# Kernel optimization log

Hardware: AMD Instinct MI355X
Metric: run time of the kernel (lower is better)

## Reference

```python
import jax, jax.numpy as jnp
import numpy as np

B, S, D = 2, 4096, 1024

def setup_inputs() -> dict:
    key = jax.random.key(0)
    k1, k2 = jax.random.split(key)
    x = jax.random.normal(k1, (B, S, D), dtype=jnp.float32)
    W = jax.random.normal(k2, (D, 3 * D), dtype=jnp.float32) * (1.0 / np.sqrt(D))
    b = jnp.zeros((3 * D,), dtype=jnp.float32)
    return {"x": x, "W": W, "b": b}

def reference(x, W, b) -> jnp.ndarray:
    D_ = x.shape[-1]
    qkv = x @ W + b                       # [B, S, 3D]
    q, k, v = jnp.split(qkv, 3, axis=2)    # each [B, S, D]
    scale = 1.0 / jnp.sqrt(jnp.asarray(D_, dtype=x.dtype))
    scores = jnp.einsum('bqd,bkd->bqk', q, k) * scale  # [B, S, S]
    weights = jax.nn.softmax(scores, axis=-1)
    return jnp.einsum('bqk,bkd->bqd', weights, v)       # [B, S, D]
```

## Files before the change

kernel.cpp:

```cpp
#include <hip/hip_runtime.h>
#include <hip/hip_bf16.h>

typedef __attribute__((ext_vector_type(4))) float  f32x4;
typedef __attribute__((ext_vector_type(8))) __bf16 bf16x8;
typedef __attribute__((ext_vector_type(8))) unsigned short u16x8;

typedef const __attribute__((address_space(1))) void gas_void;
typedef __attribute__((address_space(3))) void las_void;

__device__ __forceinline__ unsigned short f2bf(float x) {
    unsigned u = __builtin_bit_cast(unsigned, x);
    u += 0x7fffu + ((u >> 16) & 1u);
    return (unsigned short)(u >> 16);
}
__device__ __forceinline__ float bf2f(unsigned short h) {
    unsigned u = ((unsigned)h) << 16;
    return __builtin_bit_cast(float, u);
}
__device__ __forceinline__ void gload_lds16(const void* g, void* l) {
    __builtin_amdgcn_global_load_lds((gas_void*)g, (las_void*)l, 16, 0, 0);
}

__global__ void k_f32_to_bf16(const float* __restrict__ in,
                              unsigned short* __restrict__ out, int n4) {
    int i = blockIdx.x * blockDim.x + threadIdx.x;
    if (i < n4) {
        float4 v = ((const float4*)in)[i];
        ushort4 o;
        o.x = f2bf(v.x); o.y = f2bf(v.y); o.z = f2bf(v.z); o.w = f2bf(v.w);
        ((ushort4*)out)[i] = o;
    }
}

__global__ void k_transpose_w(const float* __restrict__ W,
                              unsigned short* __restrict__ Wt,
                              int K, int N) {
    __shared__ unsigned short tile[32][33];
    int n0 = blockIdx.x * 32, k0 = blockIdx.y * 32;
    int tx = threadIdx.x, ty = threadIdx.y;
#pragma unroll
    for (int i = 0; i < 4; i++) {
        int kk = ty + i * 8;
        tile[kk][tx] = f2bf(W[(size_t)(k0 + kk) * N + n0 + tx]);
    }
    __syncthreads();
#pragma unroll
    for (int i = 0; i < 4; i++) {
        int nn = ty + i * 8;
        Wt[(size_t)(n0 + nn) * K + k0 + tx] = tile[tx][nn];
    }
}

__global__ void k_transpose_v(const unsigned short* __restrict__ Vrow,
                              unsigned short* __restrict__ Vt) {
    __shared__ unsigned short tile[32][33];
    int b = blockIdx.z;
    int s0 = blockIdx.x * 32, d0 = blockIdx.y * 32;
    int tx = threadIdx.x, ty = threadIdx.y;
#pragma unroll
    for (int i = 0; i < 4; i++) {
        int ss = ty + i * 8;
        tile[ss][tx] = Vrow[((size_t)(b * 4096 + s0 + ss)) * 1024 + d0 + tx];
    }
    __syncthreads();
#pragma unroll
    for (int i = 0; i < 4; i++) {
        int dd = ty + i * 8;
        Vt[((size_t)b * 1024 + d0 + dd) * 4096 + s0 + tx] = tile[tx][dd];
    }
}

template <int MODE>
__global__ void k_gemm_bt(const unsigned short* __restrict__ A, int lda,
                          const unsigned short* __restrict__ Bt, int ldb,
                          void* __restrict__ C, int ldc,
                          unsigned short* __restrict__ Vp,
                          const float* __restrict__ bias,
                          int K, float alpha,
                          long sA, long sB, long sC) {
    __shared__ __align__(16) unsigned short As[128 * 32];
    __shared__ __align__(16) unsigned short Bs[128 * 32];

    const int z = blockIdx.z;
    A  += (size_t)z * sA;
    Bt += (size_t)z * sB;

    const int tid  = threadIdx.x;
    const int lane = tid & 63;
    const int w    = tid >> 6;
    const int wr   = w >> 1, wc = w & 1;
    const int m0   = blockIdx.y * 128;
    const int n0   = blockIdx.x * 128;

    f32x4 acc[4][4] = {};

    const int r0  = lane >> 2;
    const int cEl = (lane & 3) * 8;

    for (int k0 = 0; k0 < K; k0 += 32) {
#pragma unroll
        for (int i = 0; i < 2; i++) {
            const int c   = w + 4 * i;
            const int row = c * 16 + r0;
            gload_lds16(A + (size_t)(m0 + row) * lda + k0 + cEl,
                        (void*)(As + c * 512));
        }
#pragma unroll
        for (int i = 0; i < 2; i++) {
            const int c   = w + 4 * i;
            const int row = c * 16 + r0;
            gload_lds16(Bt + (size_t)(n0 + row) * ldb + k0 + cEl,
                        (void*)(Bs + c * 512));
        }
        __syncthreads();

        bf16x8 af[4], bfr[4];
#pragma unroll
        for (int m = 0; m < 4; m++)
            af[m] = *(const bf16x8*)&As[(wr * 64 + m * 16 + (lane & 15)) * 32 + (lane >> 4) * 8];
#pragma unroll
        for (int n = 0; n < 4; n++)
            bfr[n] = *(const bf16x8*)&Bs[(wc * 64 + n * 16 + (lane & 15)) * 32 + (lane >> 4) * 8];

#pragma unroll
        for (int m = 0; m < 4; m++)
#pragma unroll
            for (int n = 0; n < 4; n++)
                acc[m][n] = __builtin_amdgcn_mfma_f32_16x16x32_bf16(af[m], bfr[n], acc[m][n], 0, 0, 0);

        __syncthreads();
    }

#pragma unroll
    for (int m = 0; m < 4; m++) {
        const int row = m0 + wr * 64 + m * 16 + (lane >> 4) * 4;
#pragma unroll
        for (int n = 0; n < 4; n++) {
            const int col = n0 + wc * 64 + n * 16 + (lane & 15);
            const float bv = (MODE == 2) ? bias[col] : 0.0f;
#pragma unroll
            for (int r = 0; r < 4; r++) {
                const float v = acc[m][n][r] * alpha + bv;
                if (MODE == 0) {
                    ((float*)C)[(size_t)z * sC + (size_t)(row + r) * ldc + col] = v;
                } else if (MODE == 1) {
                    ((unsigned short*)C)[(size_t)z * sC + (size_t)(row + r) * ldc + col] = f2bf(v);
                } else {
                    const int lc = col & 1023;
                    if (col < 2048) {
                        ((unsigned short*)C)[(size_t)(col >> 10) * 8388608 +
                                             (size_t)(row + r) * 1024 + lc] = f2bf(v);
                    } else {
                        Vp[(size_t)(row + r) * 1024 + lc] = f2bf(v);
                    }
                }
            }
        }
    }
}

__global__ __launch_bounds__(256) void k_softmax_inplace(unsigned short* __restrict__ P, int S) {
    __shared__ float red[8];
    const int row  = blockIdx.x;
    const int tid  = threadIdx.x;
    const int lane = tid & 63;
    const int wid  = tid >> 6;
    unsigned short* p = P + (size_t)row * S;

    float v[16];
    u16x8 h0 = *(const u16x8*)&p[tid * 16];
    u16x8 h1 = *(const u16x8*)&p[tid * 16 + 8];
    float mx = -1e30f;
#pragma unroll
    for (int j = 0; j < 8; j++) { v[j]     = bf2f(h0[j]); mx = fmaxf(mx, v[j]);     }
#pragma unroll
    for (int j = 0; j < 8; j++) { v[j + 8] = bf2f(h1[j]); mx = fmaxf(mx, v[j + 8]); }

#pragma unroll
    for (int o = 32; o >= 1; o >>= 1) mx = fmaxf(mx, __shfl_xor(mx, o));
    if (lane == 0) red[wid] = mx;
    __syncthreads();
    mx = fmaxf(fmaxf(red[0], red[1]), fmaxf(red[2], red[3]));

    float sum = 0.0f;
#pragma unroll
    for (int j = 0; j < 16; j++) { v[j] = __expf(v[j] - mx); sum += v[j]; }
#pragma unroll
    for (int o = 32; o >= 1; o >>= 1) sum += __shfl_xor(sum, o);
    if (lane == 0) red[4 + wid] = sum;
    __syncthreads();
    sum = red[4] + red[5] + red[6] + red[7];
    const float rinv = 1.0f / sum;

    u16x8 o0, o1;
#pragma unroll
    for (int j = 0; j < 8; j++) { o0[j] = f2bf(v[j] * rinv); o1[j] = f2bf(v[j + 8] * rinv); }
    *(u16x8*)&p[tid * 16]     = o0;
    *(u16x8*)&p[tid * 16 + 8] = o1;
}

extern "C" void kernel_launch(void* const* d_in, const int* in_sizes, int n_in,
                              void* d_out, int out_size, void* d_ws, size_t ws_size,
                              hipStream_t stream) {
    const float* x    = (const float*)d_in[0];
    const float* W    = (const float*)d_in[1];
    const float* bias = (const float*)d_in[2];
    float* out        = (float*)d_out;

    char* ws = (char*)d_ws;
    unsigned short* Qb   = (unsigned short*)(ws);
    unsigned short* Vt   = (unsigned short*)(ws + 33554432);
    unsigned short* xb   = (unsigned short*)(ws + 50331648);
    unsigned short* Wt   = (unsigned short*)(ws + 67108864);
    unsigned short* Vrow = (unsigned short*)(ws + 73400320);
    unsigned short* Pcat = (unsigned short*)(ws + 50331648);

    k_f32_to_bf16<<<8192, 256, 0, stream>>>(x, xb, (8192 * 1024) / 4);
    k_transpose_w<<<dim3(96, 32), dim3(32, 8), 0, stream>>>(W, Wt, 1024, 3072);
    k_gemm_bt<2><<<dim3(24, 64, 1), 256, 0, stream>>>(
        xb, 1024, Wt, 1024, (void*)Qb, 1024, Vrow, bias, 1024, 1.0f, 0, 0, 0);
    k_transpose_v<<<dim3(128, 32, 2), dim3(32, 8), 0, stream>>>(Vrow, Vt);

    const float scale = 0.03125f;
    k_gemm_bt<1><<<dim3(32, 32, 2), 256, 0, stream>>>(
        Qb, 1024, Qb + 8388608, 1024, (void*)Pcat, 4096, nullptr, nullptr,
        1024, scale, 4194304, 4194304, 16777216);
    k_softmax_inplace<<<8192, 256, 0, stream>>>(Pcat, 4096);
    k_gemm_bt<0><<<dim3(8, 32, 2), 256, 0, stream>>>(
        Pcat, 4096, Vt, 4096, (void*)out, 1024, nullptr, nullptr,
        4096, 1.0f, 16777216, 4194304, 4194304);
}
```

Measured before the change: 302.6 us.

## Use 256x256 double-buffered swizzled-LDS GEMM for QKV and score products

```diff
diff --git a/kernel.cpp b/kernel.cpp
--- a/kernel.cpp
+++ b/kernel.cpp
@@ -20,6 +20,8 @@
 __device__ __forceinline__ void gload_lds16(const void* g, void* l) {
     __builtin_amdgcn_global_load_lds((gas_void*)g, (las_void*)l, 16, 0, 0);
 }
+
+#define WAITVM(N) asm volatile("s_waitcnt vmcnt(" #N ")" ::: "memory")
 
 __global__ void k_f32_to_bf16(const float* __restrict__ in,
                               unsigned short* __restrict__ out, int n4) {
@@ -71,45 +73,187 @@
 }
 
 template <int MODE>
-__global__ void k_gemm_bt(const unsigned short* __restrict__ A, int lda,
-                          const unsigned short* __restrict__ Bt, int ldb,
-                          void* __restrict__ C, int ldc,
-                          unsigned short* __restrict__ Vp,
-                          const float* __restrict__ bias,
-                          int K, float alpha,
-                          long sA, long sB, long sC) {
-    __shared__ __align__(16) unsigned short As[128 * 32];
-    __shared__ __align__(16) unsigned short Bs[128 * 32];
+__global__ __launch_bounds__(512, 2) void k_gemm256(
+        const unsigned short* __restrict__ A, int lda,
+        const unsigned short* __restrict__ Bt, int ldb,
+        void* __restrict__ C, int ldc,
+        unsigned short* __restrict__ Vp,
+        const float* __restrict__ bias,
+        int K, float alpha, long sA, long sB, long sC) {
+    __shared__ __align__(16) unsigned short As[2][16384];
+    __shared__ __align__(16) unsigned short Bs[2][16384];
 
     const int z = blockIdx.z;
     A  += (size_t)z * sA;
     Bt += (size_t)z * sB;
+
+    const int nwg  = gridDim.x * gridDim.y;
+    const int flat = blockIdx.y * gridDim.x + blockIdx.x;
+    const int swzb = (flat & 7) * (nwg >> 3) + (flat >> 3);
+    const int m0   = (swzb / gridDim.x) * 256;
+    const int n0   = (swzb % gridDim.x) * 256;
+
+    const int tid  = threadIdx.x;
+    const int lane = tid & 63;
+    const int wid  = tid >> 6;
+    const int wm   = wid >> 2;
+    const int wn   = wid & 3;
+    const int l15  = lane & 15;
+    const int l4   = lane >> 4;
+
+    f32x4 acc[8][4] = {};
+
+    auto stageA = [&](int b, int h, int kt) {
+#pragma unroll
+        for (int c = 0; c < 2; c++) {
+            int phi = c * 8192 + tid * 16;
+            int lam = phi ^ (((phi >> 9) & 1) << 5);
+            int rowp = lam >> 7;
+            int kel  = (lam & 127) >> 1;
+            int grow = m0 + (rowp >> 6) * 128 + h * 64 + (rowp & 63);
+            gload_lds16(A + (size_t)grow * lda + kt * 64 + kel,
+                        (char*)As + b * 32768 + h * 16384 + c * 8192 + (wid << 10));
+        }
+    };
+    auto stageB = [&](int b, int h, int kt) {
+#pragma unroll
+        for (int c = 0; c < 2; c++) {
+            int phi = c * 8192 + tid * 16;
+            int lam = phi ^ (((phi >> 9) & 1) << 5);
+            int rowp = lam >> 7;
+            int kel  = (lam & 127) >> 1;
+            int gnrow = n0 + (rowp >> 5) * 64 + h * 32 + (rowp & 31);
+            gload_lds16(Bt + (size_t)gnrow * ldb + kt * 64 + kel,
+                        (char*)Bs + b * 32768 + h * 16384 + c * 8192 + (wid << 10));
+        }
+    };
+    auto rdA = [&](int b, int qm, int mf, int kk) -> bf16x8 {
+        int rowp = wm * 64 + mf * 16 + l15;
+        int lam  = qm * 16384 + rowp * 128 + kk * 64 + l4 * 16;
+        int ads  = lam ^ (((lam >> 9) & 1) << 5);
+        return *(const bf16x8*)((const char*)As + b * 32768 + ads);
+    };
+    auto rdB = [&](int b, int qn, int nf, int kk) -> bf16x8 {
+        int rowp = wn * 32 + nf * 16 + l15;
+        int lam  = qn * 16384 + rowp * 128 + kk * 64 + l4 * 16;
+        int ads  = lam ^ (((lam >> 9) & 1) << 5);
+        return *(const bf16x8*)((const char*)Bs + b * 32768 + ads);
+    };
+
+#define MM(I, J, X, Y) \
+    acc[I][J] = __builtin_amdgcn_mfma_f32_16x16x32_bf16((X), (Y), acc[I][J], 0, 0, 0)
+
+#define PHASE(BUF, QM, QN, WAIT_STMT, STG_STMT)                                \
+    do {                                                                       \
+        WAIT_STMT;                                                             \
+        __builtin_amdgcn_s_barrier();                                          \
+        __builtin_amdgcn_sched_barrier(0);                                     \
+        STG_STMT;                                                              \
+        bf16x8 a00 = rdA(BUF, QM, 0, 0), a01 = rdA(BUF, QM, 0, 1);             \
+        bf16x8 a10 = rdA(BUF, QM, 1, 0), a11 = rdA(BUF, QM, 1, 1);             \
+        bf16x8 a20 = rdA(BUF, QM, 2, 0), a21 = rdA(BUF, QM, 2, 1);             \
+        bf16x8 a30 = rdA(BUF, QM, 3, 0), a31 = rdA(BUF, QM, 3, 1);             \
+        bf16x8 b00 = rdB(BUF, QN, 0, 0), b01 = rdB(BUF, QN, 0, 1);             \
+        bf16x8 b10 = rdB(BUF, QN, 1, 0), b11 = rdB(BUF, QN, 1, 1);             \
+        __builtin_amdgcn_s_setprio(1);                                         \
+        MM(QM * 4 + 0, QN * 2 + 0, a00, b00); MM(QM * 4 + 0, QN * 2 + 0, a01, b01); \
+        MM(QM * 4 + 0, QN * 2 + 1, a00, b10); MM(QM * 4 + 0, QN * 2 + 1, a01, b11); \
+        MM(QM * 4 + 1, QN * 2 + 0, a10, b00); MM(QM * 4 + 1, QN * 2 + 0, a11, b01); \
+        MM(QM * 4 + 1, QN * 2 + 1, a10, b10); MM(QM * 4 + 1, QN * 2 + 1, a11, b11); \
+        MM(QM * 4 + 2, QN * 2 + 0, a20, b00); MM(QM * 4 + 2, QN * 2 + 0, a21, b01); \
+        MM(QM * 4 + 2, QN * 2 + 1, a20, b10); MM(QM * 4 + 2, QN * 2 + 1, a21, b11); \
+        MM(QM * 4 + 3, QN * 2 + 0, a30, b00); MM(QM * 4 + 3, QN * 2 + 0, a31, b01); \
+        MM(QM * 4 + 3, QN * 2 + 1, a30, b10); MM(QM * 4 + 3, QN * 2 + 1, a31, b11); \
+        __builtin_amdgcn_s_setprio(0);                                         \
+    } while (0)
+
+    const int NT = K >> 6;
+    stageA(0, 0, 0); stageB(0, 0, 0); stageA(0, 1, 0); stageB(0, 1, 0);
+
+    for (int t = 0; t < NT; t++) {
+        const int cb = t & 1, nb = cb ^ 1;
+        if (t + 1 < NT) {
+            PHASE(cb, 0, 0, WAITVM(4), stageA(nb, 0, t + 1));
+            PHASE(cb, 1, 0, WAITVM(4), stageB(nb, 0, t + 1));
+            PHASE(cb, 0, 1, WAITVM(4), stageA(nb, 1, t + 1));
+            PHASE(cb, 1, 1, (void)0,   stageB(nb, 1, t + 1));
+        } else {
+            PHASE(cb, 0, 0, WAITVM(4), (void)0);
+            PHASE(cb, 1, 0, WAITVM(2), (void)0);
+            PHASE(cb, 0, 1, WAITVM(0), (void)0);
+            PHASE(cb, 1, 1, (void)0,   (void)0);
+        }
+    }
+#undef PHASE
+#undef MM
+
+#pragma unroll
+    for (int qm = 0; qm < 2; qm++)
+#pragma unroll
+    for (int mf = 0; mf < 4; mf++) {
+        const int row = m0 + wm * 128 + qm * 64 + mf * 16 + l4 * 4;
+#pragma unroll
+        for (int qn = 0; qn < 2; qn++)
+#pragma unroll
+        for (int nf = 0; nf < 2; nf++) {
+            const int col = n0 + wn * 64 + qn * 32 + nf * 16 + l15;
+            const float bv = (MODE == 2) ? bias[col] : 0.0f;
+            const f32x4 av = acc[qm * 4 + mf][qn * 2 + nf];
+#pragma unroll
+            for (int r = 0; r < 4; r++) {
+                const float v = av[r] * alpha + bv;
+                if (MODE == 1) {
+                    ((unsigned short*)C)[(size_t)z * sC + (size_t)(row + r) * ldc + col] = f2bf(v);
+                } else {
+                    const int lc = col & 1023;
+                    if (col < 2048)
+                        ((unsigned short*)C)[(size_t)(col >> 10) * 8388608 +
+                                             (size_t)(row + r) * 1024 + lc] = f2bf(v);
+                    else
+                        Vp[(size_t)(row + r) * 1024 + lc] = f2bf(v);
+                }
+            }
+        }
+    }
+}
+
+__global__ void k_gemm_bt_f32(const unsigned short* __restrict__ A, int lda,
+                              const unsigned short* __restrict__ Bt, int ldb,
+                              float* __restrict__ C, int ldc,
+                              int K, long sA, long sB, long sC) {
+    __shared__ __align__(16) unsigned short As[128 * 32];
+    __shared__ __align__(16) unsigned short Bs[128 * 32];
+
+    const int z = blockIdx.z;
+    A  += (size_t)z * sA;
+    Bt += (size_t)z * sB;
+
+    const int nwg  = gridDim.x * gridDim.y;
+    const int flat = blockIdx.y * gridDim.x + blockIdx.x;
+    const int swzb = (flat & 7) * (nwg >> 3) + (flat >> 3);
+    const int m0   = (swzb / gridDim.x) * 128;
+    const int n0   = (swzb % gridDim.x) * 128;
 
     const int tid  = threadIdx.x;
     const int lane = tid & 63;
     const int w    = tid >> 6;
     const int wr   = w >> 1, wc = w & 1;
-    const int m0   = blockIdx.y * 128;
-    const int n0   = blockIdx.x * 128;
 
     f32x4 acc[4][4] = {};
-
     const int r0  = lane >> 2;
     const int cEl = (lane & 3) * 8;
 
     for (int k0 = 0; k0 < K; k0 += 32) {
 #pragma unroll
         for (int i = 0; i < 2; i++) {
-            const int c   = w + 4 * i;
-            const int row = c * 16 + r0;
-            gload_lds16(A + (size_t)(m0 + row) * lda + k0 + cEl,
+            const int c = w + 4 * i;
+            gload_lds16(A + (size_t)(m0 + c * 16 + r0) * lda + k0 + cEl,
                         (void*)(As + c * 512));
         }
 #pragma unroll
         for (int i = 0; i < 2; i++) {
-            const int c   = w + 4 * i;
-            const int row = c * 16 + r0;
-            gload_lds16(Bt + (size_t)(n0 + row) * ldb + k0 + cEl,
+            const int c = w + 4 * i;
+            gload_lds16(Bt + (size_t)(n0 + c * 16 + r0) * ldb + k0 + cEl,
                         (void*)(Bs + c * 512));
         }
         __syncthreads();
@@ -137,24 +281,9 @@
 #pragma unroll
         for (int n = 0; n < 4; n++) {
             const int col = n0 + wc * 64 + n * 16 + (lane & 15);
-            const float bv = (MODE == 2) ? bias[col] : 0.0f;
-#pragma unroll
-            for (int r = 0; r < 4; r++) {
-                const float v = acc[m][n][r] * alpha + bv;
-                if (MODE == 0) {
-                    ((float*)C)[(size_t)z * sC + (size_t)(row + r) * ldc + col] = v;
-                } else if (MODE == 1) {
-                    ((unsigned short*)C)[(size_t)z * sC + (size_t)(row + r) * ldc + col] = f2bf(v);
-                } else {
-                    const int lc = col & 1023;
-                    if (col < 2048) {
-                        ((unsigned short*)C)[(size_t)(col >> 10) * 8388608 +
-                                             (size_t)(row + r) * 1024 + lc] = f2bf(v);
-                    } else {
-                        Vp[(size_t)(row + r) * 1024 + lc] = f2bf(v);
-                    }
-                }
-            }
+#pragma unroll
+            for (int r = 0; r < 4; r++)
+                C[(size_t)z * sC + (size_t)(row + r) * ldc + col] = acc[m][n][r];
         }
     }
 }
@@ -217,16 +346,15 @@
 
     k_f32_to_bf16<<<8192, 256, 0, stream>>>(x, xb, (8192 * 1024) / 4);
     k_transpose_w<<<dim3(96, 32), dim3(32, 8), 0, stream>>>(W, Wt, 1024, 3072);
-    k_gemm_bt<2><<<dim3(24, 64, 1), 256, 0, stream>>>(
+    k_gemm256<2><<<dim3(12, 32, 1), 512, 0, stream>>>(
         xb, 1024, Wt, 1024, (void*)Qb, 1024, Vrow, bias, 1024, 1.0f, 0, 0, 0);
     k_transpose_v<<<dim3(128, 32, 2), dim3(32, 8), 0, stream>>>(Vrow, Vt);
 
     const float scale = 0.03125f;
-    k_gemm_bt<1><<<dim3(32, 32, 2), 256, 0, stream>>>(
+    k_gemm256<1><<<dim3(16, 16, 2), 512, 0, stream>>>(
         Qb, 1024, Qb + 8388608, 1024, (void*)Pcat, 4096, nullptr, nullptr,
         1024, scale, 4194304, 4194304, 16777216);
     k_softmax_inplace<<<8192, 256, 0, stream>>>(Pcat, 4096);
-    k_gemm_bt<0><<<dim3(8, 32, 2), 256, 0, stream>>>(
-        Pcat, 4096, Vt, 4096, (void*)out, 1024, nullptr, nullptr,
-        4096, 1.0f, 16777216, 4194304, 4194304);
-}
+    k_gemm_bt_f32<<<dim3(8, 32, 2), 256, 0, stream>>>(
+        Pcat, 4096, Vt, 4096, out, 1024, 4096, 16777216, 4194304, 4194304);
+}
```

After: 1.005 ms. 3.32x slower.

## Double-buffer GEMM with K=64 swizzled LDS tiles and fuse V transpose into projection

Applied to the files above, without the earlier changes.

```diff
diff --git a/kernel.cpp b/kernel.cpp
--- a/kernel.cpp
+++ b/kernel.cpp
@@ -20,6 +20,9 @@
 __device__ __forceinline__ void gload_lds16(const void* g, void* l) {
     __builtin_amdgcn_global_load_lds((gas_void*)g, (las_void*)l, 16, 0, 0);
 }
+
+#define WAITVM(N) asm volatile("s_waitcnt vmcnt(" #N ")" ::: "memory")
+#define BAR() do { __builtin_amdgcn_s_barrier(); __builtin_amdgcn_sched_barrier(0); } while (0)
 
 __global__ void k_f32_to_bf16(const float* __restrict__ in,
                               unsigned short* __restrict__ out, int n4) {
@@ -51,108 +54,137 @@
     }
 }
 
-__global__ void k_transpose_v(const unsigned short* __restrict__ Vrow,
-                              unsigned short* __restrict__ Vt) {
-    __shared__ unsigned short tile[32][33];
-    int b = blockIdx.z;
-    int s0 = blockIdx.x * 32, d0 = blockIdx.y * 32;
-    int tx = threadIdx.x, ty = threadIdx.y;
-#pragma unroll
-    for (int i = 0; i < 4; i++) {
-        int ss = ty + i * 8;
-        tile[ss][tx] = Vrow[((size_t)(b * 4096 + s0 + ss)) * 1024 + d0 + tx];
-    }
-    __syncthreads();
-#pragma unroll
-    for (int i = 0; i < 4; i++) {
-        int dd = ty + i * 8;
-        Vt[((size_t)b * 1024 + d0 + dd) * 4096 + s0 + tx] = tile[tx][dd];
-    }
-}
-
 template <int MODE>
-__global__ void k_gemm_bt(const unsigned short* __restrict__ A, int lda,
-                          const unsigned short* __restrict__ Bt, int ldb,
-                          void* __restrict__ C, int ldc,
-                          unsigned short* __restrict__ Vp,
-                          const float* __restrict__ bias,
-                          int K, float alpha,
-                          long sA, long sB, long sC) {
-    __shared__ __align__(16) unsigned short As[128 * 32];
-    __shared__ __align__(16) unsigned short Bs[128 * 32];
+__global__ __launch_bounds__(256, 2) void k_g128(
+        const unsigned short* __restrict__ A, int lda,
+        const unsigned short* __restrict__ Bt, int ldb,
+        void* __restrict__ C, int ldc,
+        unsigned short* __restrict__ Vt,
+        const float* __restrict__ bias,
+        int K, float alpha, long sA, long sB, long sC) {
+    __shared__ __align__(16) unsigned short As[2][8192];
+    __shared__ __align__(16) unsigned short Bs[2][8192];
 
     const int z = blockIdx.z;
     A  += (size_t)z * sA;
     Bt += (size_t)z * sB;
 
+    const int nwg  = gridDim.x * gridDim.y;
+    const int flat = blockIdx.y * gridDim.x + blockIdx.x;
+    const int swzb = (flat & 7) * (nwg >> 3) + (flat >> 3);
+    const int m0   = (swzb / gridDim.x) * 128;
+    const int n0   = (swzb % gridDim.x) * 128;
+
     const int tid  = threadIdx.x;
     const int lane = tid & 63;
-    const int w    = tid >> 6;
-    const int wr   = w >> 1, wc = w & 1;
-    const int m0   = blockIdx.y * 128;
-    const int n0   = blockIdx.x * 128;
+    const int wid  = tid >> 6;
+    const int wr   = wid >> 1;
+    const int wc   = wid & 1;
+    const int l15  = lane & 15;
+    const int l4   = lane >> 4;
 
     f32x4 acc[4][4] = {};
 
-    const int r0  = lane >> 2;
-    const int cEl = (lane & 3) * 8;
-
-    for (int k0 = 0; k0 < K; k0 += 32) {
-#pragma unroll
-        for (int i = 0; i < 2; i++) {
-            const int c   = w + 4 * i;
-            const int row = c * 16 + r0;
-            gload_lds16(A + (size_t)(m0 + row) * lda + k0 + cEl,
-                        (void*)(As + c * 512));
+    const int srow = tid >> 3;
+    const int kel  = (((lane & 7) ^ (lane >> 3)) << 3);
+    const int c0 = (l4 << 4) ^ ((l15 & 7) << 4);
+    const int c1 = (64 + (l4 << 4)) ^ ((l15 & 7) << 4);
+
+    auto stA = [&](int b, int g, int kt) {
+        gload_lds16(A + (size_t)(m0 + g * 32 + srow) * lda + kt * 64 + kel,
+                    (char*)As + b * 16384 + g * 4096 + (wid << 10));
+    };
+    auto stB = [&](int b, int g, int kt) {
+        gload_lds16(Bt + (size_t)(n0 + g * 32 + srow) * ldb + kt * 64 + kel,
+                    (char*)Bs + b * 16384 + g * 4096 + (wid << 10));
+    };
+
+#define MM(I, J, X, Y) \
+    acc[I][J] = __builtin_amdgcn_mfma_f32_16x16x32_bf16((X), (Y), acc[I][J], 0, 0, 0)
+
+    const int NT = K >> 6;
+    stA(0, 0, 0); stA(0, 1, 0); stA(0, 2, 0); stA(0, 3, 0);
+    stB(0, 0, 0); stB(0, 1, 0); stB(0, 2, 0); stB(0, 3, 0);
+
+    for (int t = 0; t < NT; t++) {
+        const int cur = t & 1, nxt = cur ^ 1;
+        const char* Ab = (const char*)As + cur * 16384;
+        const char* Bb = (const char*)Bs + cur * 16384;
+        const bool hn = (t + 1 < NT);
+
+        bf16x8 af[4], bq[4];
+
+        if (hn) {
+            stA(nxt, 0, t + 1); stA(nxt, 1, t + 1); stA(nxt, 2, t + 1); stA(nxt, 3, t + 1);
+            WAITVM(4);
+        } else {
+            WAITVM(0);
         }
-#pragma unroll
-        for (int i = 0; i < 2; i++) {
-            const int c   = w + 4 * i;
-            const int row = c * 16 + r0;
-            gload_lds16(Bt + (size_t)(n0 + row) * ldb + k0 + cEl,
-                        (void*)(Bs + c * 512));
+        BAR();
+#pragma unroll
+        for (int mf = 0; mf < 4; mf++)
+            af[mf] = *(const bf16x8*)(Ab + (wr * 64 + mf * 16 + l15) * 128 + c0);
+#pragma unroll
+        for (int nf = 0; nf < 4; nf++)
+            bq[nf] = *(const bf16x8*)(Bb + (wc * 64 + nf * 16 + l15) * 128 + c0);
+        __builtin_amdgcn_s_setprio(1);
+#pragma unroll
+        for (int mf = 0; mf < 4; mf++)
+#pragma unroll
+        for (int nf = 0; nf < 4; nf++)
+            MM(mf, nf, af[mf], bq[nf]);
+        __builtin_amdgcn_s_setprio(0);
+
+        if (hn) {
+            stB(nxt, 0, t + 1); stB(nxt, 1, t + 1); stB(nxt, 2, t + 1); stB(nxt, 3, t + 1);
         }
-        __syncthreads();
-
-        bf16x8 af[4], bfr[4];
-#pragma unroll
-        for (int m = 0; m < 4; m++)
-            af[m] = *(const bf16x8*)&As[(wr * 64 + m * 16 + (lane & 15)) * 32 + (lane >> 4) * 8];
-#pragma unroll
-        for (int n = 0; n < 4; n++)
-            bfr[n] = *(const bf16x8*)&Bs[(wc * 64 + n * 16 + (lane & 15)) * 32 + (lane >> 4) * 8];
-
-#pragma unroll
-        for (int m = 0; m < 4; m++)
-#pragma unroll
-            for (int n = 0; n < 4; n++)
-                acc[m][n] = __builtin_amdgcn_mfma_f32_16x16x32_bf16(af[m], bfr[n], acc[m][n], 0, 0, 0);
-
-        __syncthreads();
-    }
-
-#pragma unroll
-    for (int m = 0; m < 4; m++) {
-        const int row = m0 + wr * 64 + m * 16 + (lane >> 4) * 4;
-#pragma unroll
-        for (int n = 0; n < 4; n++) {
-            const int col = n0 + wc * 64 + n * 16 + (lane & 15);
-            const float bv = (MODE == 2) ? bias[col] : 0.0f;
-#pragma unroll
-            for (int r = 0; r < 4; r++) {
-                const float v = acc[m][n][r] * alpha + bv;
-                if (MODE == 0) {
-                    ((float*)C)[(size_t)z * sC + (size_t)(row + r) * ldc + col] = v;
-                } else if (MODE == 1) {
-                    ((unsigned short*)C)[(size_t)z * sC + (size_t)(row + r) * ldc + col] = f2bf(v);
+#pragma unroll
+        for (int mf = 0; mf < 4; mf++)
+            af[mf] = *(const bf16x8*)(Ab + (wr * 64 + mf * 16 + l15) * 128 + c1);
+#pragma unroll
+        for (int nf = 0; nf < 4; nf++)
+            bq[nf] = *(const bf16x8*)(Bb + (wc * 64 + nf * 16 + l15) * 128 + c1);
+        __builtin_amdgcn_s_setprio(1);
+#pragma unroll
+        for (int mf = 0; mf < 4; mf++)
+#pragma unroll
+        for (int nf = 0; nf < 4; nf++)
+            MM(mf, nf, af[mf], bq[nf]);
+        __builtin_amdgcn_s_setprio(0);
+        BAR();
+    }
+#undef MM
+
+#pragma unroll
+    for (int mf = 0; mf < 4; mf++) {
+        const int row = m0 + wr * 64 + mf * 16 + l4 * 4;
+#pragma unroll
+        for (int nf = 0; nf < 4; nf++) {
+            const int col = n0 + wc * 64 + nf * 16 + l15;
+            const f32x4 av = acc[mf][nf];
+            if (MODE == 0) {
+#pragma unroll
+                for (int r = 0; r < 4; r++)
+                    ((float*)C)[(size_t)z * sC + (size_t)(row + r) * ldc + col] = av[r];
+            } else if (MODE == 1) {
+#pragma unroll
+                for (int r = 0; r < 4; r++)
+                    ((unsigned short*)C)[(size_t)z * sC + (size_t)(row + r) * ldc + col]
+                        = f2bf(av[r] * alpha);
+            } else {
+                const float bv = bias[col];
+                const int lc = col & 1023;
+                if (col < 2048) {
+#pragma unroll
+                    for (int r = 0; r < 4; r++)
+                        ((unsigned short*)C)[(size_t)(col >> 10) * 8388608 +
+                                             (size_t)(row + r) * 1024 + lc] = f2bf(av[r] + bv);
                 } else {
-                    const int lc = col & 1023;
-                    if (col < 2048) {
-                        ((unsigned short*)C)[(size_t)(col >> 10) * 8388608 +
-                                             (size_t)(row + r) * 1024 + lc] = f2bf(v);
-                    } else {
-                        Vp[(size_t)(row + r) * 1024 + lc] = f2bf(v);
-                    }
+                    const int b = row >> 12, s = row & 4095;
+                    ushort4 o;
+                    o.x = f2bf(av[0] + bv); o.y = f2bf(av[1] + bv);
+                    o.z = f2bf(av[2] + bv); o.w = f2bf(av[3] + bv);
+                    *(ushort4*)&Vt[(size_t)b * 4194304 + (size_t)lc * 4096 + s] = o;
                 }
             }
         }
@@ -212,21 +244,19 @@
     unsigned short* Vt   = (unsigned short*)(ws + 33554432);
     unsigned short* xb   = (unsigned short*)(ws + 50331648);
     unsigned short* Wt   = (unsigned short*)(ws + 67108864);
-    unsigned short* Vrow = (unsigned short*)(ws + 73400320);
     unsigned short* Pcat = (unsigned short*)(ws + 50331648);
 
     k_f32_to_bf16<<<8192, 256, 0, stream>>>(x, xb, (8192 * 1024) / 4);
     k_transpose_w<<<dim3(96, 32), dim3(32, 8), 0, stream>>>(W, Wt, 1024, 3072);
-    k_gemm_bt<2><<<dim3(24, 64, 1), 256, 0, stream>>>(
-        xb, 1024, Wt, 1024, (void*)Qb, 1024, Vrow, bias, 1024, 1.0f, 0, 0, 0);
-    k_transpose_v<<<dim3(128, 32, 2), dim3(32, 8), 0, stream>>>(Vrow, Vt);
+    k_g128<2><<<dim3(24, 64, 1), 256, 0, stream>>>(
+        xb, 1024, Wt, 1024, (void*)Qb, 1024, Vt, bias, 1024, 1.0f, 0, 0, 0);
 
     const float scale = 0.03125f;
-    k_gemm_bt<1><<<dim3(32, 32, 2), 256, 0, stream>>>(
+    k_g128<1><<<dim3(32, 32, 2), 256, 0, stream>>>(
         Qb, 1024, Qb + 8388608, 1024, (void*)Pcat, 4096, nullptr, nullptr,
         1024, scale, 4194304, 4194304, 16777216);
     k_softmax_inplace<<<8192, 256, 0, stream>>>(Pcat, 4096);
-    k_gemm_bt<0><<<dim3(8, 32, 2), 256, 0, stream>>>(
+    k_g128<0><<<dim3(8, 32, 2), 256, 0, stream>>>(
         Pcat, 4096, Vt, 4096, (void*)out, 1024, nullptr, nullptr,
         4096, 1.0f, 16777216, 4194304, 4194304);
 }
```

After: 304.1 us. Within noise of the previous version (+0.5%).
